# Performance work log

Measured on AMD Instinct MI355X. Metric: run time of the kernel, lower is better.

## Reference

```python
import jax, jax.numpy as jnp
import numpy as np

B, S, T, H, E, VIN, VOUT = 2048, 24, 25, 256, 300, 64, 128


def gru_cell(x, h, Wih, Whh, bih, bhh):
    # PyTorch GRU gate order: r, z, n
    gi = x @ Wih + bih          # [B, 3H]
    gh = h @ Whh + bhh          # [B, 3H]
    hd = h.shape[-1]
    ir, iz, in_ = gi[:, :hd], gi[:, hd:2 * hd], gi[:, 2 * hd:]
    hr, hz, hn = gh[:, :hd], gh[:, hd:2 * hd], gh[:, 2 * hd:]
    r = jax.nn.sigmoid(ir + hr)
    z = jax.nn.sigmoid(iz + hz)
    n = jnp.tanh(in_ + r * hn)
    return (1.0 - z) * n + z * h


def setup_inputs() -> dict:
    key = jax.random.key(0)
    ks = jax.random.split(key, 26)
    it = iter(range(26))

    def p(shape):
        return jax.random.normal(ks[next(it)], shape, jnp.float32) * 0.05

    src = jax.random.randint(ks[next(it)], (S, B), 0, VIN)
    trg = jax.random.randint(ks[next(it)], (T, B), 0, VOUT)
    return dict(
        src=src, trg=trg,
        enc_emb=p((VIN, E)),
        enc_Wih_f=p((E, 3 * H)), enc_Whh_f=p((H, 3 * H)), enc_bih_f=p((3 * H,)), enc_bhh_f=p((3 * H,)),
        enc_Wih_b=p((E, 3 * H)), enc_Whh_b=p((H, 3 * H)), enc_bih_b=p((3 * H,)), enc_bhh_b=p((3 * H,)),
        enc_fcW=p((2 * H, H)), enc_fcb=p((H,)),
        attn_Wh=p((H, H)), attn_We=p((2 * H, H)), attn_b=p((H,)), attn_v=p((H,)),
        dec_emb=p((VOUT, E)),
        dec_Wih=p((E + 2 * H, 3 * H)), dec_Whh=p((H, 3 * H)), dec_bih=p((3 * H,)), dec_bhh=p((3 * H,)),
        fcW=p((H + 2 * H + E, VOUT)), fcb=p((VOUT,)),
        teacher_forcing_ratio=1,
    )


def reference(src, trg, enc_emb, enc_Wih_f, enc_Whh_f, enc_bih_f, enc_bhh_f,
              enc_Wih_b, enc_Whh_b, enc_bih_b, enc_bhh_b, enc_fcW, enc_fcb,
              attn_Wh, attn_We, attn_b, attn_v, dec_emb,
              dec_Wih, dec_Whh, dec_bih, dec_bhh, fcW, fcb,
              teacher_forcing_ratio):
    # ---- Encoder: bidirectional single-layer GRU ----
    x = enc_emb[src]                                   # [S, B, E]
    h0 = jnp.zeros((x.shape[1], H), x.dtype)

    def mk(Wih, Whh, bih, bhh):
        def step(h, xt):
            hn = gru_cell(xt, h, Wih, Whh, bih, bhh)
            return hn, hn
        return step

    hf, out_f = jax.lax.scan(mk(enc_Wih_f, enc_Whh_f, enc_bih_f, enc_bhh_f), h0, x)
    hb, out_b = jax.lax.scan(mk(enc_Wih_b, enc_Whh_b, enc_bih_b, enc_bhh_b), h0, x[::-1])
    enc_out = jnp.concatenate([out_f, out_b[::-1]], axis=-1)   # [S, B, 2H]
    hidden = jnp.tanh(jnp.concatenate([hf, hb], axis=-1) @ enc_fcW + enc_fcb)  # [B, H]

    # ---- Decoder: teacher-forced loop (teacher_forcing_ratio=1 => deterministic) ----
    enc_bse = enc_out.transpose(1, 0, 2)               # [B, S, 2H]
    enc_proj = enc_bse @ attn_We                       # [B, S, H] (hoisted linear part of attn)
    embed_seq = dec_emb[trg[:-1]]                      # [T-1, B, E]

    def dec_step(h, emb_t):
        energy = jnp.tanh((h @ attn_Wh)[:, None, :] + enc_proj + attn_b)  # [B, S, H]
        a = jax.nn.softmax(energy @ attn_v, axis=-1)                      # [B, S]
        weighted = jnp.einsum('bs,bsd->bd', a, enc_bse)                   # [B, 2H]
        xg = jnp.concatenate([emb_t, weighted], axis=-1)                  # [B, E+2H]
        hn = gru_cell(xg, h, dec_Wih, dec_Whh, dec_bih, dec_bhh)          # [B, H]
        logits = jnp.concatenate([hn, weighted, emb_t], axis=-1) @ fcW + fcb
        return hn, logits

    _, logits = jax.lax.scan(dec_step, hidden, embed_seq)  # [T-1, B, VOUT]
    outputs = jnp.concatenate(
        [jnp.zeros((1,) + logits.shape[1:], logits.dtype), logits], axis=0)  # [T, B, VOUT]
    return outputs
```

## Files before the change

kernel.cpp:

```cpp
#include <hip/hip_runtime.h>
#include <hip/hip_bf16.h>

typedef __hip_bfloat16 bf16;
typedef __attribute__((ext_vector_type(8))) short short8;
typedef __attribute__((ext_vector_type(4))) short short4v;
typedef __attribute__((ext_vector_type(4))) float f32x4;

#define MFMA(va, vb, vc) \
  __builtin_amdgcn_mfma_f32_16x16x32_bf16(va, vb, vc, 0, 0, 0)

__device__ __forceinline__ float to_f(float x) { return x; }
__device__ __forceinline__ float to_f(bf16 x) { return __bfloat162float(x); }
__device__ __forceinline__ float ldp(const void* p, size_t i, bool f32) {
  return f32 ? ((const float*)p)[i] : __bfloat162float(((const bf16*)p)[i]);
}
__device__ __forceinline__ short f2b(float f) {
  bf16 h = __float2bfloat16(f);
  return *reinterpret_cast<short*>(&h);
}
__device__ __forceinline__ float b2f(short s_) {
  unsigned int ui = ((unsigned int)(unsigned short)s_) << 16;
  float f;
  __builtin_memcpy(&f, &ui, 4);
  return f;
}
__device__ __forceinline__ int perm1024(int c) {
  return ((c & 255) >> 4) * 64 + (c >> 8) * 16 + (c & 15);
}

__global__ void detect_kernel(const void* __restrict__ probe,
                              unsigned* __restrict__ flag) {
  __shared__ int sbad;
  if (threadIdx.x == 0) sbad = 0;
  __syncthreads();
  const unsigned short* u = (const unsigned short*)probe;
  int bad = 0;
  for (int i = threadIdx.x; i < 2048; i += 256) {
    unsigned short w = u[i];
    unsigned e = (w >> 7) & 0xFFu;
    bool plaus = (w == 0) || (w == 0x8000u) || (e >= 0x60u && e <= 0x7Eu);
    if (!plaus) bad++;
  }
  atomicAdd(&sbad, bad);
  __syncthreads();
  if (threadIdx.x == 0) *flag = (sbad > 100) ? 1u : 0u;
}

#define MAXSEG 24
struct PrepArgs {
  int nseg;
  const void* src[MAXSEG];
  long long soff[MAXSEG];
  short* dst[MAXSEG];
  int scols[MAXSEG];
  int dstride[MAXSEG];
  int transp[MAXSEG];
  long long prefix[MAXSEG + 1];
};
__global__ void prep_kernel(PrepArgs a, const unsigned* __restrict__ dflag) {
  const bool isf32 = (*dflag != 0u);
  long long i = (long long)blockIdx.x * 256 + threadIdx.x;
  if (i >= a.prefix[a.nseg]) return;
  int s = 0;
  while (i >= a.prefix[s + 1]) s++;
  long long loc = i - a.prefix[s];
  long long r = loc / a.scols[s], c = loc % a.scols[s];
  float v = a.src[s] ? ldp(a.src[s], (size_t)(a.soff[s] + loc), isf32) : 0.f;
  int tp = a.transp[s];
  long long idx;
  if (tp == 1)
    idx = c * a.dstride[s] + r;
  else if (tp == 2)
    idx = (long long)perm1024((int)c) * a.dstride[s] + r;
  else if (tp == 3)
    idx = perm1024((int)c);
  else
    idx = r * a.dstride[s] + c;
  a.dst[s][idx] = f2b(v);
}

struct GJob {
  const bf16* A;
  const short* WT;
  const bf16* bias;
  float* Cf;
  bf16* Ch;
  const float* Cin;
  const int* cinrow;
  int lda, wst, K, M, N, flags;
};
struct GJobs {
  GJob j[4];
};

__global__ __launch_bounds__(256) void mj_gemm(GJobs args) {
  GJob jb = args.j[blockIdx.z];
  const int n0 = blockIdx.x * 128, m0 = blockIdx.y * 128;
  if (n0 >= jb.N || m0 >= jb.M) return;
  __shared__ short As[128][40];
  __shared__ short Bs[128][40];
  const int tid = threadIdx.x, lane = tid & 63, wave = tid >> 6;
  const int srow = tid >> 1, skoff = (tid & 1) * 16;
  const int wr = (wave >> 1) * 64, wc = (wave & 1) * 64;

  const short* abase =
      (const short*)jb.A + (long long)(m0 + srow) * jb.lda + skoff;
  const short* bbase = jb.WT + (long long)(n0 + srow) * jb.wst + skoff;
  f32x4 acc[4][4];
#pragma unroll
  for (int i = 0; i < 4; i++)
#pragma unroll
    for (int j = 0; j < 4; j++) acc[i][j] = 0.f;

  short8 a0 = *(const short8*)(abase);
  short8 a1 = *(const short8*)(abase + 8);
  short8 b0 = *(const short8*)(bbase);
  short8 b1 = *(const short8*)(bbase + 8);
  for (int k0 = 0; k0 < jb.K; k0 += 32) {
    __syncthreads();
    *(short8*)&As[srow][skoff] = a0;
    *(short8*)&As[srow][skoff + 8] = a1;
    *(short8*)&Bs[srow][skoff] = b0;
    *(short8*)&Bs[srow][skoff + 8] = b1;
    __syncthreads();
    int kn = (k0 + 32 < jb.K) ? k0 + 32 : k0;
    a0 = *(const short8*)(abase + kn);
    a1 = *(const short8*)(abase + kn + 8);
    b0 = *(const short8*)(bbase + kn);
    b1 = *(const short8*)(bbase + kn + 8);
    short8 af[4], bfr[4];
#pragma unroll
    for (int i = 0; i < 4; i++)
      af[i] = *(short8*)&As[wr + i * 16 + (lane & 15)][(lane >> 4) * 8];
#pragma unroll
    for (int j = 0; j < 4; j++)
      bfr[j] = *(short8*)&Bs[wc + j * 16 + (lane & 15)][(lane >> 4) * 8];
#pragma unroll
    for (int i = 0; i < 4; i++)
#pragma unroll
      for (int j = 0; j < 4; j++) acc[i][j] = MFMA(af[i], bfr[j], acc[i][j]);
  }
  const int N = jb.N;
  const float* cin = jb.Cin;
  const int* cri = jb.cinrow;
#pragma unroll
  for (int j = 0; j < 4; j++) {
    int col = n0 + wc + j * 16 + (lane & 15);
    float bv = jb.bias ? to_f(jb.bias[col]) : 0.f;
#pragma unroll
    for (int i = 0; i < 4; i++) {
#pragma unroll
      for (int r = 0; r < 4; r++) {
        int row = m0 + wr + i * 16 + (lane >> 4) * 4 + r;
        float v = acc[i][j][r] + bv;
        if (cin) {
          long long crow = cri ? (long long)cri[row] : (long long)row;
          v += cin[crow * N + col];
        }
        if (jb.flags & 4) v = tanhf(v);
        if (jb.Cf) jb.Cf[(long long)row * N + col] = v;
        if (jb.Ch) jb.Ch[(long long)row * N + col] = __float2bfloat16(v);
      }
    }
  }
}

struct CJob {
  const bf16* A;
  const short* WT;
  const bf16* bias;
  const int* tok;
  const bf16* giTab;
  float* hF;
  bf16* hBf;
  bf16* out2;
  long long out2s;
  int lda, wst, K, hstride, hoff;
};
struct CJobs {
  CJob j[2];
};

__global__ __launch_bounds__(256) void mj_gemm_cell(CJobs args) {
  CJob jb = args.j[blockIdx.z];
  const int n0 = blockIdx.x * 128, m0 = blockIdx.y * 128;
  __shared__ short As[128][40];
  __shared__ short Bs[128][40];
  __shared__ int toks[128];
  const int tid = threadIdx.x, lane = tid & 63, wave = tid >> 6;
  const int srow = tid >> 1, skoff = (tid & 1) * 16;
  const int wr = (wave >> 1) * 64, wcq = (wave & 1) * 64;

  if (tid < 128) toks[tid] = jb.tok[m0 + tid];
  const short* abase =
      (const short*)jb.A + (long long)(m0 + srow) * jb.lda + skoff;
  const short* bbase = jb.WT + (long long)(n0 + srow) * jb.wst + skoff;

  f32x4 acc[4][4];
#pragma unroll
  for (int i = 0; i < 4; i++)
#pragma unroll
    for (int j = 0; j < 4; j++) acc[i][j] = 0.f;

  short8 a0 = *(const short8*)(abase);
  short8 a1 = *(const short8*)(abase + 8);
  short8 b0 = *(const short8*)(bbase);
  short8 b1 = *(const short8*)(bbase + 8);
  for (int k0 = 0; k0 < jb.K; k0 += 32) {
    __syncthreads();
    *(short8*)&As[srow][skoff] = a0;
    *(short8*)&As[srow][skoff + 8] = a1;
    *(short8*)&Bs[srow][skoff] = b0;
    *(short8*)&Bs[srow][skoff + 8] = b1;
    __syncthreads();
    int kn = (k0 + 32 < jb.K) ? k0 + 32 : k0;
    a0 = *(const short8*)(abase + kn);
    a1 = *(const short8*)(abase + kn + 8);
    b0 = *(const short8*)(bbase + kn);
    b1 = *(const short8*)(bbase + kn + 8);
    short8 af[4], bfr[4];
#pragma unroll
    for (int i = 0; i < 4; i++)
      af[i] = *(short8*)&As[wr + i * 16 + (lane & 15)][(lane >> 4) * 8];
#pragma unroll
    for (int j = 0; j < 4; j++)
      bfr[j] = *(short8*)&Bs[wcq + j * 16 + (lane & 15)][(lane >> 4) * 8];
#pragma unroll
    for (int i = 0; i < 4; i++)
#pragma unroll
      for (int j = 0; j < 4; j++) acc[i][j] = MFMA(af[i], bfr[j], acc[i][j]);
  }

  const int u = lane & 15, hi4 = (lane >> 4) * 4;
  const int i_h = ((n0 + wcq) >> 6) * 16 + u;
  const float b0g = to_f(jb.bias[n0 + wcq + u]);
  const float b1g = to_f(jb.bias[n0 + wcq + 16 + u]);
  const float b2g = to_f(jb.bias[n0 + wcq + 32 + u]);
#pragma unroll
  for (int i = 0; i < 4; i++) {
#pragma unroll
    for (int r = 0; r < 4; r++) {
      int row = m0 + wr + i * 16 + hi4 + r;
      const bf16* gi = jb.giTab + (long long)toks[row - m0] * 768 + i_h;
      float ir = to_f(gi[0]), iz = to_f(gi[256]), in_ = to_f(gi[512]);
      float hr = acc[i][0][r] + b0g;
      float hz = acc[i][1][r] + b1g;
      float hn = acc[i][2][r] + b2g;
      long long hidx = (long long)row * jb.hstride + jb.hoff + i_h;
      float hv = jb.hF[hidx];
      float rr = 1.f / (1.f + expf(-(ir + hr)));
      float zz = 1.f / (1.f + expf(-(iz + hz)));
      float nn = tanhf(in_ + rr * hn);
      float o = (1.f - zz) * nn + zz * hv;
      jb.hF[hidx] = o;
      jb.hBf[hidx] = __float2bfloat16(o);
      jb.out2[(long long)row * jb.out2s + i_h] = __float2bfloat16(o);
    }
  }
}

struct A3Args {
  const bf16* hwh;
  const bf16* proj;
  const bf16* bse;
  const void* v;
  const unsigned* dflag;
  bf16* xr;
};
__global__ __launch_bounds__(256) void attn3_kernel(A3Args a) {
  const int b = blockIdx.x, tid = threadIdx.x;
  const int wave = tid >> 6, lane = tid & 63;
  __shared__ float esc[24];
  __shared__ float aw[24];
  const bool isf32 = (*a.dflag != 0u);
  float vv[4], hw[4];
  {
    short4v h4 =
        *(const short4v*)((const short*)a.hwh + (size_t)b * 256 + lane * 4);
#pragma unroll
    for (int e = 0; e < 4; e++) {
      hw[e] = b2f(h4[e]);
      vv[e] = ldp(a.v, lane * 4 + e, isf32);
    }
  }
  const short* pb = (const short*)a.proj + (size_t)b * 6144 + lane * 4;
  short4v p4s[6];
#pragma unroll
  for (int i = 0; i < 6; i++)
    p4s[i] = *(const short4v*)(pb + (wave * 6 + i) * 256);
#pragma unroll
  for (int i = 0; i < 6; i++) {
    float t = 0.f;
#pragma unroll
    for (int e = 0; e < 4; e++)
      t += vv[e] * tanhf(hw[e] + b2f(p4s[i][e]));
#pragma unroll
    for (int off = 1; off < 64; off <<= 1) t += __shfl_xor(t, off, 64);
    if (lane == 0) esc[wave * 6 + i] = t;
  }
  __syncthreads();
  if (wave == 0) {
    float xv = (lane < 24) ? esc[lane] : -1e30f;
    float mx = xv;
#pragma unroll
    for (int off = 1; off < 64; off <<= 1)
      mx = fmaxf(mx, __shfl_xor(mx, off, 64));
    float e = (lane < 24) ? expf(xv - mx) : 0.f;
    float sm = e;
#pragma unroll
    for (int off = 1; off < 64; off <<= 1) sm += __shfl_xor(sm, off, 64);
    if (lane < 24) aw[lane] = e / sm;
  }
  __syncthreads();
  const short* eb = (const short*)a.bse + (size_t)b * 12288 + tid * 2;
  float w0 = 0.f, w1 = 0.f;
#pragma unroll
  for (int s = 0; s < 24; s++) {
    unsigned q = *(const unsigned*)(eb + s * 512);
    float aa = aw[s];
    w0 += aa * b2f((short)(q & 0xffff));
    w1 += aa * b2f((short)(q >> 16));
  }
  unsigned o = ((unsigned)(unsigned short)f2b(w1) << 16) |
               (unsigned)(unsigned short)f2b(w0);
  *(unsigned*)((short*)a.xr + (size_t)b * 768 + tid * 2) = o;
}

struct C2Args {
  const bf16* xr;
  const bf16* hprev;
  const short* W7p;
  const short* WhhP;
  const bf16* bhhP;
  const int* tok;
  const bf16* giTabE;
  float* hF;
  bf16* hnext;
  bf16* xout;
};

__device__ __forceinline__ void tile_acc3(const short* abase,
                                          const short* bbase, int K,
                                          short (*As)[40], short (*Bs)[40],
                                          int srow, int skoff, int wr,
                                          int wcq, int lane, f32x4 acc[4][3]) {
  short8 a0 = *(const short8*)(abase);
  short8 a1 = *(const short8*)(abase + 8);
  short8 b0 = *(const short8*)(bbase);
  short8 b1 = *(const short8*)(bbase + 8);
  for (int k0 = 0; k0 < K; k0 += 32) {
    __syncthreads();
    *(short8*)&As[srow][skoff] = a0;
    *(short8*)&As[srow][skoff + 8] = a1;
    *(short8*)&Bs[srow][skoff] = b0;
    *(short8*)&Bs[srow][skoff + 8] = b1;
    __syncthreads();
    int kn = (k0 + 32 < K) ? k0 + 32 : k0;
    a0 = *(const short8*)(abase + kn);
    a1 = *(const short8*)(abase + kn + 8);
    b0 = *(const short8*)(bbase + kn);
    b1 = *(const short8*)(bbase + kn + 8);
    short8 af[4], bfr[3];
#pragma unroll
    for (int i = 0; i < 4; i++)
      af[i] = *(short8*)&As[wr + i * 16 + (lane & 15)][(lane >> 4) * 8];
#pragma unroll
    for (int j = 0; j < 3; j++)
      bfr[j] = *(short8*)&Bs[wcq + j * 16 + (lane & 15)][(lane >> 4) * 8];
#pragma unroll
    for (int i = 0; i < 4; i++)
#pragma unroll
      for (int j = 0; j < 3; j++) acc[i][j] = MFMA(af[i], bfr[j], acc[i][j]);
  }
}

__global__ __launch_bounds__(256) void cell2_kernel(C2Args a) {
  const int n0 = blockIdx.x * 128, m0 = blockIdx.y * 128;
  __shared__ short As[128][40];
  __shared__ short Bs[128][40];
  __shared__ int toks[128];
  const int tid = threadIdx.x, lane = tid & 63, wave = tid >> 6;
  const int srow = tid >> 1, skoff = (tid & 1) * 16;
  const int wr = (wave >> 1) * 64, wcq = (wave & 1) * 64;
  if (tid < 128) toks[tid] = a.tok[m0 + tid];

  f32x4 accA[4][3], accB[4][3];
#pragma unroll
  for (int i = 0; i < 4; i++)
#pragma unroll
    for (int j = 0; j < 3; j++) {
      accA[i][j] = 0.f;
      accB[i][j] = 0.f;
    }
  tile_acc3((const short*)a.xr + (long long)(m0 + srow) * 768 + skoff,
            a.W7p + (long long)(n0 + srow) * 512 + skoff, 512, As, Bs, srow,
            skoff, wr, wcq, lane, accA);
  tile_acc3((const short*)a.hprev + (long long)(m0 + srow) * 256 + skoff,
            a.WhhP + (long long)(n0 + srow) * 256 + skoff, 256, As, Bs, srow,
            skoff, wr, wcq, lane, accB);

  const int u = lane & 15, hi4 = (lane >> 4) * 4;
  const int i_h = ((n0 + wcq) >> 6) * 16 + u;
  const float b0g = to_f(a.bhhP[n0 + wcq + u]);
  const float b1g = to_f(a.bhhP[n0 + wcq + 16 + u]);
  const float b2g = to_f(a.bhhP[n0 + wcq + 32 + u]);
#pragma unroll
  for (int i = 0; i < 4; i++) {
#pragma unroll
    for (int r = 0; r < 4; r++) {
      int row = m0 + wr + i * 16 + hi4 + r;
      const bf16* gi = a.giTabE + (long long)toks[row - m0] * 768 + i_h;
      float ir = accA[i][0][r] + to_f(gi[0]);
      float iz = accA[i][1][r] + to_f(gi[256]);
      float in_ = accA[i][2][r] + to_f(gi[512]);
      float hr = accB[i][0][r] + b0g;
      float hz = accB[i][1][r] + b1g;
      float hn = accB[i][2][r] + b2g;
      long long hidx = (long long)row * 256 + i_h;
      float hv = a.hF[hidx];
      float rr = 1.f / (1.f + expf(-(ir + hr)));
      float zz = 1.f / (1.f + expf(-(iz + hz)));
      float nn = tanhf(in_ + rr * hn);
      float o = (1.f - zz) * nn + zz * hv;
      a.hF[hidx] = o;
      a.hnext[hidx] = __float2bfloat16(o);
      a.xout[(long long)row * 768 + 512 + i_h] = __float2bfloat16(o);
    }
  }
}

__global__ void sentinel_kernel(float* out, int n) {
  int i = blockIdx.x * 256 + threadIdx.x;
  if (i < n) out[i] = 123.0f;
}

extern "C" void kernel_launch(void* const* d_in, const int* in_sizes, int n_in,
                              void* d_out, int out_size, void* d_ws,
                              size_t ws_size, hipStream_t stream) {
  const int B = 2048, S = 24, T = 25, VOUT = 128;
  const int* src = (const int*)d_in[0];
  const int* trg = (const int*)d_in[1];
  const void* enc_emb = d_in[2];
  const void* enc_Wih_f = d_in[3];
  const void* enc_Whh_f = d_in[4];
  const void* enc_bih_f = d_in[5];
  const void* enc_bhh_f = d_in[6];
  const void* enc_Wih_b = d_in[7];
  const void* enc_Whh_b = d_in[8];
  const void* enc_bih_b = d_in[9];
  const void* enc_bhh_b = d_in[10];
  const void* enc_fcW = d_in[11];
  const void* enc_fcb = d_in[12];
  const void* attn_Wh = d_in[13];
  const void* attn_We = d_in[14];
  const void* attn_b = d_in[15];
  const void* attn_v = d_in[16];
  const void* dec_emb = d_in[17];
  const void* dec_Wih = d_in[18];
  const void* dec_Whh = d_in[19];
  const void* dec_bih = d_in[20];
  const void* dec_bhh = d_in[21];
  const void* fcW = d_in[22];
  const void* fcb = d_in[23];
  float* out = (float*)d_out;

  size_t need = 0;
  auto place = [&](size_t bytes) {
    size_t off = need;
    need += (bytes + 255) & ~(size_t)255;
    return off;
  };
  size_t o_flag = place(256);
  size_t o_wstart = need;
  size_t oEmbE = place(64 * 320 * 2);
  size_t oEmbD = place(128 * 320 * 2);
  size_t oWT1 = place(768 * 320 * 2);
  size_t oWT2 = place(1024 * 256 * 2);
  size_t oWT3 = place(768 * 320 * 2);
  size_t oWT4 = place(1024 * 256 * 2);
  size_t oWT5 = place(256 * 512 * 2);
  size_t oWT6 = place(256 * 512 * 2);
  size_t oWhhP = place(1024 * 256 * 2);
  size_t oWhT = place(256 * 256 * 2);
  size_t oW7aT = place(768 * 320 * 2);
  size_t oW7bT = place(1024 * 512 * 2);
  size_t oW8aT = place(128 * 320 * 2);
  size_t oW8bT = place(128 * 768 * 2);
  size_t oB1 = place(768 * 2), oB2 = place(1024 * 2);
  size_t oB3 = place(768 * 2), oB4 = place(1024 * 2);
  size_t oB5 = place(256 * 2), oB6 = place(256 * 2);
  size_t oB7 = place(768 * 2), oBcP = place(1024 * 2), oB8 = place(128 * 2);
  size_t o_wend = need;
  size_t o_bse = place((size_t)B * S * 512 * 2);
  size_t o_proj = place((size_t)B * S * 256 * 2);
  size_t o_xgc = place((size_t)(T - 1) * B * 768 * 2);
  size_t o_hfb = place((size_t)B * 512 * 4);
  size_t o_hb0 = place((size_t)B * 512 * 2);
  size_t o_hb1 = place((size_t)B * 512 * 2);
  size_t o_hd = place((size_t)B * 256 * 4);
  size_t o_hdb0 = place((size_t)B * 256 * 2);
  size_t o_hdb1 = place((size_t)B * 256 * 2);
  size_t o_hwh = place((size_t)B * 256 * 2);
  size_t o_gtF = place(128 * 768 * 2);
  size_t o_gtB = place(128 * 768 * 2);
  size_t o_gtE = place(128 * 768 * 2);
  size_t o_fcT = place(128 * 128 * 4);

  if (ws_size < need) {
    sentinel_kernel<<<(out_size + 255) / 256, 256, 0, stream>>>(out, out_size);
    return;
  }

  char* base = (char*)d_ws;
  unsigned* dflag = (unsigned*)(base + o_flag);
  bf16* embE = (bf16*)(base + oEmbE);
  bf16* embD = (bf16*)(base + oEmbD);
  short* WT1 = (short*)(base + oWT1);
  short* WT2p = (short*)(base + oWT2);
  short* WT3 = (short*)(base + oWT3);
  short* WT4p = (short*)(base + oWT4);
  short* WT5 = (short*)(base + oWT5);
  short* WT6 = (short*)(base + oWT6);
  short* WhhP = (short*)(base + oWhhP);
  short* WhT = (short*)(base + oWhT);
  short* W7aT = (short*)(base + oW7aT);
  short* W7bTp = (short*)(base + oW7bT);
  short* W8aT = (short*)(base + oW8aT);
  short* W8bT = (short*)(base + oW8bT);
  bf16 *B1 = (bf16*)(base + oB1), *B2p = (bf16*)(base + oB2);
  bf16 *B3 = (bf16*)(base + oB3), *B4p = (bf16*)(base + oB4);
  bf16 *B5 = (bf16*)(base + oB5), *B6 = (bf16*)(base + oB6);
  bf16 *B7 = (bf16*)(base + oB7), *BcP = (bf16*)(base + oBcP);
  bf16* B8 = (bf16*)(base + oB8);
  bf16* bse = (bf16*)(base + o_bse);
  bf16* proj = (bf16*)(base + o_proj);
  bf16* xgcAll = (bf16*)(base + o_xgc);
  float* hfb = (float*)(base + o_hfb);
  bf16* hb[2] = {(bf16*)(base + o_hb0), (bf16*)(base + o_hb1)};
  float* h_d = (float*)(base + o_hd);
  bf16* hdbf[2] = {(bf16*)(base + o_hdb0), (bf16*)(base + o_hdb1)};
  bf16* hwh = (bf16*)(base + o_hwh);
  bf16* giTabF = (bf16*)(base + o_gtF);
  bf16* giTabB = (bf16*)(base + o_gtB);
  bf16* giTabE = (bf16*)(base + o_gtE);
  float* fcTab = (float*)(base + o_fcT);

  detect_kernel<<<1, 256, 0, stream>>>(enc_emb, dflag);
  (void)hipMemsetAsync(base + o_wstart, 0, o_wend - o_wstart, stream);

  PrepArgs pa;
  int ns = 0;
  long long tot = 0;
  auto seg = [&](const void* s, long long soff, short* dst, int scols,
                 int dstride, int transp, long long count) {
    pa.src[ns] = s;
    pa.soff[ns] = soff;
    pa.dst[ns] = dst;
    pa.scols[ns] = scols;
    pa.dstride[ns] = dstride;
    pa.transp[ns] = transp;
    pa.prefix[ns] = tot;
    tot += count;
    ns++;
  };
  seg(enc_emb, 0, (short*)embE, 300, 320, 0, 64 * 300);
  seg(dec_emb, 0, (short*)embD, 300, 320, 0, 128 * 300);
  seg(enc_Wih_f, 0, WT1, 768, 320, 1, 230400);
  seg(enc_Whh_f, 0, WT2p, 768, 256, 2, 196608);
  seg(enc_Wih_b, 0, WT3, 768, 320, 1, 230400);
  seg(enc_Whh_b, 0, WT4p, 768, 256, 2, 196608);
  seg(enc_fcW, 0, WT5, 256, 512, 1, 131072);
  seg(attn_We, 0, WT6, 256, 512, 1, 131072);
  seg(dec_Whh, 0, WhhP, 768, 256, 2, 196608);
  seg(attn_Wh, 0, WhT, 256, 256, 1, 65536);
  seg(dec_Wih, 0, W7aT, 768, 320, 1, 300 * 768);
  seg(dec_Wih, (long long)300 * 768, W7bTp, 768, 512, 2, 512 * 768);
  seg(fcW, (long long)768 * 128, W8aT, 128, 320, 1, 300 * 128);
  seg(fcW, (long long)256 * 128, W8bT, 128, 768, 1, 512 * 128);
  seg(fcW, 0, W8bT + 512, 128, 768, 1, 256 * 128);
  seg(enc_bih_f, 0, (short*)B1, 768, 768, 0, 768);
  seg(enc_bhh_f, 0, (short*)B2p, 768, 1024, 3, 768);
  seg(enc_bih_b, 0, (short*)B3, 768, 768, 0, 768);
  seg(enc_bhh_b, 0, (short*)B4p, 768, 1024, 3, 768);
  seg(enc_fcb, 0, (short*)B5, 256, 256, 0, 256);
  seg(attn_b, 0, (short*)B6, 256, 256, 0, 256);
  seg(dec_bih, 0, (short*)B7, 768, 768, 0, 768);
  seg(dec_bhh, 0, (short*)BcP, 768, 1024, 3, 768);
  seg(fcb, 0, (short*)B8, 128, 128, 0, 128);
  pa.prefix[ns] = tot;
  pa.nseg = ns;
  prep_kernel<<<(int)((tot + 255) / 256), 256, 0, stream>>>(pa, dflag);

  (void)hipMemsetAsync(hfb, 0, (size_t)B * 512 * 4, stream);
  (void)hipMemsetAsync(hb[0], 0, (size_t)B * 512 * 2, stream);
  (void)hipMemsetAsync(out, 0, (size_t)B * VOUT * 4, stream);

  auto launch = [&](const GJob* jobs, int nj, int gx, int gy) {
    GJobs a{};
    for (int i = 0; i < nj; i++) a.j[i] = jobs[i];
    mj_gemm<<<dim3(gx, gy, nj), 256, 0, stream>>>(a);
  };

  {
    GJob tj[4];
    tj[0] = {embE, WT1, B1, nullptr, giTabF, nullptr, nullptr,
             320, 320, 320, 128, 768, 0};
    tj[1] = {embE, WT3, B3, nullptr, giTabB, nullptr, nullptr,
             320, 320, 320, 128, 768, 0};
    tj[2] = {embD, W7aT, B7, nullptr, giTabE, nullptr, nullptr,
             320, 320, 320, 128, 768, 0};
    tj[3] = {embD, W8aT, B8, fcTab, nullptr, nullptr, nullptr,
             320, 320, 320, 128, 128, 0};
    launch(tj, 4, 6, 1);
  }

  for (int s = 0; s < S; s++) {
    CJobs ca{};
    ca.j[0] = {hb[s & 1], WT2p, B2p, src + (size_t)s * B, giTabF,
               hfb, hb[(s + 1) & 1], bse + (size_t)s * 512, 12288,
               512, 256, 256, 512, 0};
    ca.j[1] = {hb[s & 1] + 256, WT4p, B4p, src + (size_t)(S - 1 - s) * B,
               giTabB, hfb, hb[(s + 1) & 1],
               bse + (size_t)(S - 1 - s) * 512 + 256, 12288,
               512, 256, 256, 512, 256};
    mj_gemm_cell<<<dim3(8, 16, 2), 256, 0, stream>>>(ca);
  }

  {
    GJob mj[2];
    mj[0] = {hb[0], WT5, B5, h_d, hdbf[0], nullptr, nullptr,
             512, 512, 512, B, 256, 4};
    mj[1] = {bse, WT6, B6, nullptr, proj, nullptr, nullptr,
             512, 512, 512, B * S, 256, 0};
    launch(mj, 2, 2, 384);
  }

  for (int t = 0; t < T - 1; t++) {
    bf16* xr = xgcAll + (size_t)t * B * 768;
    GJob jh = {hdbf[t & 1], WhT, nullptr, nullptr, hwh, nullptr, nullptr,
               256, 256, 256, B, 256, 0};
    launch(&jh, 1, 2, 16);
    A3Args aa{hwh, proj, bse, attn_v, dflag, xr};
    attn3_kernel<<<B, 256, 0, stream>>>(aa);
    C2Args cc{xr,    hdbf[t & 1], W7bTp, WhhP, BcP,
              trg + (size_t)t * B, giTabE, h_d, hdbf[(t + 1) & 1], xr};
    cell2_kernel<<<dim3(8, 16), 256, 0, stream>>>(cc);
  }

  {
    GJob jf = {xgcAll, W8bT, nullptr, out + (size_t)B * VOUT, nullptr,
               fcTab, trg, 768, 768, 768, (T - 1) * B, 128, 0};
    launch(&jf, 1, 1, 384);
  }
}
```

Measured before the change: 1.840 ms.

## Fuse attention h@Wh projection into attention kernel, four batch rows per block

```diff
diff --git a/kernel.cpp b/kernel.cpp
--- a/kernel.cpp
+++ b/kernel.cpp
@@ -259,48 +259,69 @@
   }
 }
 
-struct A3Args {
-  const bf16* hwh;
+struct A4Args {
+  const bf16* h;
+  const short* WhK;
   const bf16* proj;
   const bf16* bse;
   const void* v;
   const unsigned* dflag;
   bf16* xr;
 };
-__global__ __launch_bounds__(256) void attn3_kernel(A3Args a) {
-  const int b = blockIdx.x, tid = threadIdx.x;
+__global__ __launch_bounds__(256) void attn4_kernel(A4Args a) {
+  const int b0 = blockIdx.x * 4, tid = threadIdx.x;
   const int wave = tid >> 6, lane = tid & 63;
-  __shared__ float esc[24];
-  __shared__ float aw[24];
+  __shared__ short hsh[4][256];
+  __shared__ float hwL[4][256];
+  __shared__ float esc[4][24];
+  __shared__ float aw[4][24];
   const bool isf32 = (*a.dflag != 0u);
-  float vv[4], hw[4];
   {
-    short4v h4 =
-        *(const short4v*)((const short*)a.hwh + (size_t)b * 256 + lane * 4);
+    int r = tid >> 6, c4 = (tid & 63) * 4;
+    *(short4v*)&hsh[r][c4] =
+        *(const short4v*)((const short*)a.h + (size_t)(b0 + r) * 256 + c4);
+  }
+  __syncthreads();
+  {
+    float a0 = 0.f, a1 = 0.f, a2 = 0.f, a3 = 0.f;
+    for (int k = 0; k < 256; k++) {
+      float w = b2f(a.WhK[k * 256 + tid]);
+      a0 += w * b2f(hsh[0][k]);
+      a1 += w * b2f(hsh[1][k]);
+      a2 += w * b2f(hsh[2][k]);
+      a3 += w * b2f(hsh[3][k]);
+    }
+    hwL[0][tid] = a0;
+    hwL[1][tid] = a1;
+    hwL[2][tid] = a2;
+    hwL[3][tid] = a3;
+  }
+  __syncthreads();
+  {
+    float vv[4], hw4[4];
 #pragma unroll
     for (int e = 0; e < 4; e++) {
-      hw[e] = b2f(h4[e]);
       vv[e] = ldp(a.v, lane * 4 + e, isf32);
-    }
-  }
-  const short* pb = (const short*)a.proj + (size_t)b * 6144 + lane * 4;
-  short4v p4s[6];
-#pragma unroll
-  for (int i = 0; i < 6; i++)
-    p4s[i] = *(const short4v*)(pb + (wave * 6 + i) * 256);
-#pragma unroll
-  for (int i = 0; i < 6; i++) {
-    float t = 0.f;
-#pragma unroll
-    for (int e = 0; e < 4; e++)
-      t += vv[e] * tanhf(hw[e] + b2f(p4s[i][e]));
-#pragma unroll
-    for (int off = 1; off < 64; off <<= 1) t += __shfl_xor(t, off, 64);
-    if (lane == 0) esc[wave * 6 + i] = t;
+      hw4[e] = hwL[wave][lane * 4 + e];
+    }
+    const short* pb =
+        (const short*)a.proj + (size_t)(b0 + wave) * 6144 + lane * 4;
+    short4v p4s[24];
+#pragma unroll
+    for (int s = 0; s < 24; s++) p4s[s] = *(const short4v*)(pb + s * 256);
+#pragma unroll
+    for (int s = 0; s < 24; s++) {
+      float t = 0.f;
+#pragma unroll
+      for (int e = 0; e < 4; e++) t += vv[e] * tanhf(hw4[e] + b2f(p4s[s][e]));
+#pragma unroll
+      for (int off = 1; off < 64; off <<= 1) t += __shfl_xor(t, off, 64);
+      if (lane == 0) esc[wave][s] = t;
+    }
   }
   __syncthreads();
-  if (wave == 0) {
-    float xv = (lane < 24) ? esc[lane] : -1e30f;
+  {
+    float xv = (lane < 24) ? esc[wave][lane] : -1e30f;
     float mx = xv;
 #pragma unroll
     for (int off = 1; off < 64; off <<= 1)
@@ -309,21 +330,24 @@
     float sm = e;
 #pragma unroll
     for (int off = 1; off < 64; off <<= 1) sm += __shfl_xor(sm, off, 64);
-    if (lane < 24) aw[lane] = e / sm;
+    if (lane < 24) aw[wave][lane] = e / sm;
   }
   __syncthreads();
-  const short* eb = (const short*)a.bse + (size_t)b * 12288 + tid * 2;
-  float w0 = 0.f, w1 = 0.f;
-#pragma unroll
-  for (int s = 0; s < 24; s++) {
-    unsigned q = *(const unsigned*)(eb + s * 512);
-    float aa = aw[s];
-    w0 += aa * b2f((short)(q & 0xffff));
-    w1 += aa * b2f((short)(q >> 16));
-  }
-  unsigned o = ((unsigned)(unsigned short)f2b(w1) << 16) |
-               (unsigned)(unsigned short)f2b(w0);
-  *(unsigned*)((short*)a.xr + (size_t)b * 768 + tid * 2) = o;
+#pragma unroll
+  for (int r = 0; r < 4; r++) {
+    const short* eb = (const short*)a.bse + (size_t)(b0 + r) * 12288 + tid * 2;
+    float w0 = 0.f, w1 = 0.f;
+#pragma unroll
+    for (int s = 0; s < 24; s++) {
+      unsigned q = *(const unsigned*)(eb + s * 512);
+      float aa = aw[r][s];
+      w0 += aa * b2f((short)(q & 0xffff));
+      w1 += aa * b2f((short)(q >> 16));
+    }
+    unsigned o = ((unsigned)(unsigned short)f2b(w1) << 16) |
+                 (unsigned)(unsigned short)f2b(w0);
+    *(unsigned*)((short*)a.xr + (size_t)(b0 + r) * 768 + tid * 2) = o;
+  }
 }
 
 struct C2Args {
@@ -481,7 +505,7 @@
   size_t oWT5 = place(256 * 512 * 2);
   size_t oWT6 = place(256 * 512 * 2);
   size_t oWhhP = place(1024 * 256 * 2);
-  size_t oWhT = place(256 * 256 * 2);
+  size_t oWhK = place(256 * 256 * 2);
   size_t oW7aT = place(768 * 320 * 2);
   size_t oW7bT = place(1024 * 512 * 2);
   size_t oW8aT = place(128 * 320 * 2);
@@ -500,7 +524,6 @@
   size_t o_hd = place((size_t)B * 256 * 4);
   size_t o_hdb0 = place((size_t)B * 256 * 2);
   size_t o_hdb1 = place((size_t)B * 256 * 2);
-  size_t o_hwh = place((size_t)B * 256 * 2);
   size_t o_gtF = place(128 * 768 * 2);
   size_t o_gtB = place(128 * 768 * 2);
   size_t o_gtE = place(128 * 768 * 2);
@@ -522,7 +545,7 @@
   short* WT5 = (short*)(base + oWT5);
   short* WT6 = (short*)(base + oWT6);
   short* WhhP = (short*)(base + oWhhP);
-  short* WhT = (short*)(base + oWhT);
+  short* WhK = (short*)(base + oWhK);
   short* W7aT = (short*)(base + oW7aT);
   short* W7bTp = (short*)(base + oW7bT);
   short* W8aT = (short*)(base + oW8aT);
@@ -539,7 +562,6 @@
   bf16* hb[2] = {(bf16*)(base + o_hb0), (bf16*)(base + o_hb1)};
   float* h_d = (float*)(base + o_hd);
   bf16* hdbf[2] = {(bf16*)(base + o_hdb0), (bf16*)(base + o_hdb1)};
-  bf16* hwh = (bf16*)(base + o_hwh);
   bf16* giTabF = (bf16*)(base + o_gtF);
   bf16* giTabB = (bf16*)(base + o_gtB);
   bf16* giTabE = (bf16*)(base + o_gtE);
@@ -572,7 +594,7 @@
   seg(enc_fcW, 0, WT5, 256, 512, 1, 131072);
   seg(attn_We, 0, WT6, 256, 512, 1, 131072);
   seg(dec_Whh, 0, WhhP, 768, 256, 2, 196608);
-  seg(attn_Wh, 0, WhT, 256, 256, 1, 65536);
+  seg(attn_Wh, 0, WhK, 256, 256, 0, 65536);
   seg(dec_Wih, 0, W7aT, 768, 320, 1, 300 * 768);
   seg(dec_Wih, (long long)300 * 768, W7bTp, 768, 512, 2, 512 * 768);
   seg(fcW, (long long)768 * 128, W8aT, 128, 320, 1, 300 * 128);
@@ -637,11 +659,8 @@
 
   for (int t = 0; t < T - 1; t++) {
     bf16* xr = xgcAll + (size_t)t * B * 768;
-    GJob jh = {hdbf[t & 1], WhT, nullptr, nullptr, hwh, nullptr, nullptr,
-               256, 256, 256, B, 256, 0};
-    launch(&jh, 1, 2, 16);
-    A3Args aa{hwh, proj, bse, attn_v, dflag, xr};
-    attn3_kernel<<<B, 256, 0, stream>>>(aa);
+    A4Args aa{hdbf[t & 1], WhK, proj, bse, attn_v, dflag, xr};
+    attn4_kernel<<<512, 256, 0, stream>>>(aa);
     C2Args cc{xr,    hdbf[t & 1], W7bTp, WhhP, BcP,
               trg + (size_t)t * B, giTabE, h_d, hdbf[(t + 1) & 1], xr};
     cell2_kernel<<<dim3(8, 16), 256, 0, stream>>>(cc);
```

Measured after the change: 2.140 ms. 1.16x slower.

## Fuse decoder h@Whh into attention-projection GEMM, drop recurrent GEMM from cell kernel

Applied to the files above, without the earlier changes.

```diff
diff --git a/kernel.cpp b/kernel.cpp
--- a/kernel.cpp
+++ b/kernel.cpp
@@ -260,7 +260,7 @@
 }
 
 struct A3Args {
-  const bf16* hwh;
+  const bf16* ghw;
   const bf16* proj;
   const bf16* bse;
   const void* v;
@@ -275,8 +275,8 @@
   const bool isf32 = (*a.dflag != 0u);
   float vv[4], hw[4];
   {
-    short4v h4 =
-        *(const short4v*)((const short*)a.hwh + (size_t)b * 256 + lane * 4);
+    short4v h4 = *(const short4v*)((const short*)a.ghw + (size_t)b * 1280 +
+                                   1024 + lane * 4);
 #pragma unroll
     for (int e = 0; e < 4; e++) {
       hw[e] = b2f(h4[e]);
@@ -326,11 +326,10 @@
   *(unsigned*)((short*)a.xr + (size_t)b * 768 + tid * 2) = o;
 }
 
-struct C2Args {
+struct C3Args {
   const bf16* xr;
-  const bf16* hprev;
+  const bf16* ghw;
   const short* W7p;
-  const short* WhhP;
   const bf16* bhhP;
   const int* tok;
   const bf16* giTabE;
@@ -339,42 +338,7 @@
   bf16* xout;
 };
 
-__device__ __forceinline__ void tile_acc3(const short* abase,
-                                          const short* bbase, int K,
-                                          short (*As)[40], short (*Bs)[40],
-                                          int srow, int skoff, int wr,
-                                          int wcq, int lane, f32x4 acc[4][3]) {
-  short8 a0 = *(const short8*)(abase);
-  short8 a1 = *(const short8*)(abase + 8);
-  short8 b0 = *(const short8*)(bbase);
-  short8 b1 = *(const short8*)(bbase + 8);
-  for (int k0 = 0; k0 < K; k0 += 32) {
-    __syncthreads();
-    *(short8*)&As[srow][skoff] = a0;
-    *(short8*)&As[srow][skoff + 8] = a1;
-    *(short8*)&Bs[srow][skoff] = b0;
-    *(short8*)&Bs[srow][skoff + 8] = b1;
-    __syncthreads();
-    int kn = (k0 + 32 < K) ? k0 + 32 : k0;
-    a0 = *(const short8*)(abase + kn);
-    a1 = *(const short8*)(abase + kn + 8);
-    b0 = *(const short8*)(bbase + kn);
-    b1 = *(const short8*)(bbase + kn + 8);
-    short8 af[4], bfr[3];
-#pragma unroll
-    for (int i = 0; i < 4; i++)
-      af[i] = *(short8*)&As[wr + i * 16 + (lane & 15)][(lane >> 4) * 8];
-#pragma unroll
-    for (int j = 0; j < 3; j++)
-      bfr[j] = *(short8*)&Bs[wcq + j * 16 + (lane & 15)][(lane >> 4) * 8];
-#pragma unroll
-    for (int i = 0; i < 4; i++)
-#pragma unroll
-      for (int j = 0; j < 3; j++) acc[i][j] = MFMA(af[i], bfr[j], acc[i][j]);
-  }
-}
-
-__global__ __launch_bounds__(256) void cell2_kernel(C2Args a) {
+__global__ __launch_bounds__(256) void cell3_kernel(C3Args a) {
   const int n0 = blockIdx.x * 128, m0 = blockIdx.y * 128;
   __shared__ short As[128][40];
   __shared__ short Bs[128][40];
@@ -384,20 +348,45 @@
   const int wr = (wave >> 1) * 64, wcq = (wave & 1) * 64;
   if (tid < 128) toks[tid] = a.tok[m0 + tid];
 
-  f32x4 accA[4][3], accB[4][3];
+  f32x4 acc[4][3];
 #pragma unroll
   for (int i = 0; i < 4; i++)
 #pragma unroll
-    for (int j = 0; j < 3; j++) {
-      accA[i][j] = 0.f;
-      accB[i][j] = 0.f;
+    for (int j = 0; j < 3; j++) acc[i][j] = 0.f;
+
+  {
+    const short* abase =
+        (const short*)a.xr + (long long)(m0 + srow) * 768 + skoff;
+    const short* bbase = a.W7p + (long long)(n0 + srow) * 512 + skoff;
+    short8 a0 = *(const short8*)(abase);
+    short8 a1 = *(const short8*)(abase + 8);
+    short8 b0 = *(const short8*)(bbase);
+    short8 b1 = *(const short8*)(bbase + 8);
+    for (int k0 = 0; k0 < 512; k0 += 32) {
+      __syncthreads();
+      *(short8*)&As[srow][skoff] = a0;
+      *(short8*)&As[srow][skoff + 8] = a1;
+      *(short8*)&Bs[srow][skoff] = b0;
+      *(short8*)&Bs[srow][skoff + 8] = b1;
+      __syncthreads();
+      int kn = (k0 + 32 < 512) ? k0 + 32 : k0;
+      a0 = *(const short8*)(abase + kn);
+      a1 = *(const short8*)(abase + kn + 8);
+      b0 = *(const short8*)(bbase + kn);
+      b1 = *(const short8*)(bbase + kn + 8);
+      short8 af[4], bfr[3];
+#pragma unroll
+      for (int i = 0; i < 4; i++)
+        af[i] = *(short8*)&As[wr + i * 16 + (lane & 15)][(lane >> 4) * 8];
+#pragma unroll
+      for (int j = 0; j < 3; j++)
+        bfr[j] = *(short8*)&Bs[wcq + j * 16 + (lane & 15)][(lane >> 4) * 8];
+#pragma unroll
+      for (int i = 0; i < 4; i++)
+#pragma unroll
+        for (int j = 0; j < 3; j++) acc[i][j] = MFMA(af[i], bfr[j], acc[i][j]);
     }
-  tile_acc3((const short*)a.xr + (long long)(m0 + srow) * 768 + skoff,
-            a.W7p + (long long)(n0 + srow) * 512 + skoff, 512, As, Bs, srow,
-            skoff, wr, wcq, lane, accA);
-  tile_acc3((const short*)a.hprev + (long long)(m0 + srow) * 256 + skoff,
-            a.WhhP + (long long)(n0 + srow) * 256 + skoff, 256, As, Bs, srow,
-            skoff, wr, wcq, lane, accB);
+  }
 
   const int u = lane & 15, hi4 = (lane >> 4) * 4;
   const int i_h = ((n0 + wcq) >> 6) * 16 + u;
@@ -410,12 +399,13 @@
     for (int r = 0; r < 4; r++) {
       int row = m0 + wr + i * 16 + hi4 + r;
       const bf16* gi = a.giTabE + (long long)toks[row - m0] * 768 + i_h;
-      float ir = accA[i][0][r] + to_f(gi[0]);
-      float iz = accA[i][1][r] + to_f(gi[256]);
-      float in_ = accA[i][2][r] + to_f(gi[512]);
-      float hr = accB[i][0][r] + b0g;
-      float hz = accB[i][1][r] + b1g;
-      float hn = accB[i][2][r] + b2g;
+      const bf16* gb = a.ghw + (long long)row * 1280 + (n0 + wcq) + u;
+      float ir = acc[i][0][r] + to_f(gi[0]);
+      float iz = acc[i][1][r] + to_f(gi[256]);
+      float in_ = acc[i][2][r] + to_f(gi[512]);
+      float hr = to_f(gb[0]) + b0g;
+      float hz = to_f(gb[16]) + b1g;
+      float hn = to_f(gb[32]) + b2g;
       long long hidx = (long long)row * 256 + i_h;
       float hv = a.hF[hidx];
       float rr = 1.f / (1.f + expf(-(ir + hr)));
@@ -480,8 +470,7 @@
   size_t oWT4 = place(1024 * 256 * 2);
   size_t oWT5 = place(256 * 512 * 2);
   size_t oWT6 = place(256 * 512 * 2);
-  size_t oWhhP = place(1024 * 256 * 2);
-  size_t oWhT = place(256 * 256 * 2);
+  size_t oWcK = place(1280 * 256 * 2);
   size_t oW7aT = place(768 * 320 * 2);
   size_t oW7bT = place(1024 * 512 * 2);
   size_t oW8aT = place(128 * 320 * 2);
@@ -500,7 +489,7 @@
   size_t o_hd = place((size_t)B * 256 * 4);
   size_t o_hdb0 = place((size_t)B * 256 * 2);
   size_t o_hdb1 = place((size_t)B * 256 * 2);
-  size_t o_hwh = place((size_t)B * 256 * 2);
+  size_t o_ghw = place((size_t)B * 1280 * 2);
   size_t o_gtF = place(128 * 768 * 2);
   size_t o_gtB = place(128 * 768 * 2);
   size_t o_gtE = place(128 * 768 * 2);
@@ -521,8 +510,7 @@
   short* WT4p = (short*)(base + oWT4);
   short* WT5 = (short*)(base + oWT5);
   short* WT6 = (short*)(base + oWT6);
-  short* WhhP = (short*)(base + oWhhP);
-  short* WhT = (short*)(base + oWhT);
+  short* WcK = (short*)(base + oWcK);
   short* W7aT = (short*)(base + oW7aT);
   short* W7bTp = (short*)(base + oW7bT);
   short* W8aT = (short*)(base + oW8aT);
@@ -539,7 +527,7 @@
   bf16* hb[2] = {(bf16*)(base + o_hb0), (bf16*)(base + o_hb1)};
   float* h_d = (float*)(base + o_hd);
   bf16* hdbf[2] = {(bf16*)(base + o_hdb0), (bf16*)(base + o_hdb1)};
-  bf16* hwh = (bf16*)(base + o_hwh);
+  bf16* ghw = (bf16*)(base + o_ghw);
   bf16* giTabF = (bf16*)(base + o_gtF);
   bf16* giTabB = (bf16*)(base + o_gtB);
   bf16* giTabE = (bf16*)(base + o_gtE);
@@ -571,8 +559,8 @@
   seg(enc_Whh_b, 0, WT4p, 768, 256, 2, 196608);
   seg(enc_fcW, 0, WT5, 256, 512, 1, 131072);
   seg(attn_We, 0, WT6, 256, 512, 1, 131072);
-  seg(dec_Whh, 0, WhhP, 768, 256, 2, 196608);
-  seg(attn_Wh, 0, WhT, 256, 256, 1, 65536);
+  seg(dec_Whh, 0, WcK, 768, 256, 2, 196608);
+  seg(attn_Wh, 0, WcK + 1024 * 256, 256, 256, 1, 65536);
   seg(dec_Wih, 0, W7aT, 768, 320, 1, 300 * 768);
   seg(dec_Wih, (long long)300 * 768, W7bTp, 768, 512, 2, 512 * 768);
   seg(fcW, (long long)768 * 128, W8aT, 128, 320, 1, 300 * 128);
@@ -637,14 +625,14 @@
 
   for (int t = 0; t < T - 1; t++) {
     bf16* xr = xgcAll + (size_t)t * B * 768;
-    GJob jh = {hdbf[t & 1], WhT, nullptr, nullptr, hwh, nullptr, nullptr,
-               256, 256, 256, B, 256, 0};
-    launch(&jh, 1, 2, 16);
-    A3Args aa{hwh, proj, bse, attn_v, dflag, xr};
+    GJob jw = {hdbf[t & 1], WcK, nullptr, nullptr, ghw, nullptr, nullptr,
+               256, 256, 256, B, 1280, 0};
+    launch(&jw, 1, 10, 16);
+    A3Args aa{ghw, proj, bse, attn_v, dflag, xr};
     attn3_kernel<<<B, 256, 0, stream>>>(aa);
-    C2Args cc{xr,    hdbf[t & 1], W7bTp, WhhP, BcP,
-              trg + (size_t)t * B, giTabE, h_d, hdbf[(t + 1) & 1], xr};
-    cell2_kernel<<<dim3(8, 16), 256, 0, stream>>>(cc);
+    C3Args cc{xr, ghw, W7bTp, BcP, trg + (size_t)t * B, giTabE,
+              h_d, hdbf[(t + 1) & 1], xr};
+    cell3_kernel<<<dim3(8, 16), 256, 0, stream>>>(cc);
   }
 
   {
```

New measurement: 1.794 ms. 2.5% less time.
